# Performance work log

Measured on AMD Instinct MI355X. Metric: run time of the kernel, lower is better.

Reference implementation:

```python
import jax, jax.numpy as jnp
import numpy as np

D_MODEL = 1024
HEADS = 16
D_HEAD = D_MODEL // HEADS
LN_EPS = 1e-6


def setup_inputs() -> dict:
    key = jax.random.key(0)
    ks = jax.random.split(key, 7)
    B, S = 4, 2048
    scale = 1.0 / np.sqrt(D_MODEL)
    return {
        "q": jax.random.normal(ks[0], (B, S, D_MODEL), jnp.float32),
        "k": jax.random.normal(ks[1], (B, S, D_MODEL), jnp.float32),
        "v": jax.random.normal(ks[2], (B, S, D_MODEL), jnp.float32),
        "Wq": jax.random.normal(ks[3], (D_MODEL, D_MODEL), jnp.float32) * scale,
        "Wk": jax.random.normal(ks[4], (D_MODEL, D_MODEL), jnp.float32) * scale,
        "Wv": jax.random.normal(ks[5], (D_MODEL, D_MODEL), jnp.float32) * scale,
        "Wo": jax.random.normal(ks[6], (D_MODEL, D_MODEL), jnp.float32) * scale,
        "ln_gamma": jnp.ones((D_MODEL,), jnp.float32),
        "ln_beta": jnp.zeros((D_MODEL,), jnp.float32),
    }


def reference(q, k, v, Wq, Wk, Wv, Wo, ln_gamma, ln_beta):
    B, S, _ = q.shape
    residual = q
    # torch Linear (no bias): y = x @ W.T
    qh = (q @ Wq.T).reshape(B, S, HEADS, D_HEAD).transpose(0, 2, 1, 3)
    kh = (k @ Wk.T).reshape(B, S, HEADS, D_HEAD).transpose(0, 2, 1, 3)
    vh = (v @ Wv.T).reshape(B, S, HEADS, D_HEAD).transpose(0, 2, 1, 3)
    # scaled dot-product attention (no mask, dropout=0)
    att = jnp.einsum("bhsd,bhtd->bhst", qh, kh) / jnp.sqrt(jnp.float32(D_HEAD))
    att = jax.nn.softmax(att, axis=-1)
    ctx = jnp.einsum("bhst,bhtd->bhsd", att, vh)  # (B,H,S,Dh)
    ctx = ctx.transpose(0, 2, 1, 3).reshape(B, S, D_MODEL)
    out = ctx @ Wo.T
    out = out + residual
    # LayerNorm, eps=1e-6
    mu = out.mean(axis=-1, keepdims=True)
    var = out.var(axis=-1, keepdims=True)
    out = (out - mu) * jax.lax.rsqrt(var + LN_EPS) * ln_gamma + ln_beta
    return out
```

## Files before the change

### kernel.cpp

```cpp
#include <hip/hip_runtime.h>
#include <hip/hip_bf16.h>

#define DEVI __device__ __forceinline__

typedef unsigned int u32;
typedef unsigned short u16;
typedef __bf16 bf16_t;
typedef bf16_t bf16x8 __attribute__((ext_vector_type(8)));
typedef bf16_t bf16x4 __attribute__((ext_vector_type(4)));
typedef float f32x4 __attribute__((ext_vector_type(4)));
typedef u32 u32x4 __attribute__((ext_vector_type(4)));
typedef u32 u32x2 __attribute__((ext_vector_type(2)));

DEVI u16 f2bf(float f) {
    u32 u = __builtin_bit_cast(u32, f);
    u = (u + 0x7FFFu + ((u >> 16) & 1u)) >> 16;
    return (u16)u;
}

DEVI u32 pack2bf(float lo, float hi) {
#if __has_builtin(__builtin_amdgcn_cvt_pk_bf16_f32)
    typedef __bf16 bf16x2_t __attribute__((ext_vector_type(2)));
    return __builtin_bit_cast(u32, __builtin_amdgcn_cvt_pk_bf16_f32(lo, hi));
#else
    return (u32)f2bf(lo) | ((u32)f2bf(hi) << 16);
#endif
}

DEVI float fast_exp2(float x) { return __builtin_amdgcn_exp2f(x); }

DEVI f32x4 mfma16x16x16(bf16x4 a, bf16x4 b, f32x4 c) {
#if __has_builtin(__builtin_amdgcn_mfma_f32_16x16x16bf16_1k)
    typedef short s16x4 __attribute__((ext_vector_type(4)));
    return __builtin_amdgcn_mfma_f32_16x16x16bf16_1k(
        __builtin_bit_cast(s16x4, a), __builtin_bit_cast(s16x4, b), c, 0, 0, 0);
#else
    asm volatile("s_nop 1\n\tv_mfma_f32_16x16x16_bf16 %0, %1, %2, %0\n\ts_nop 7\n\ts_nop 3"
                 : "+v"(c) : "v"(a), "v"(b));
    return c;
#endif
}

typedef __attribute__((address_space(3))) u32 as3_u32;
typedef __attribute__((address_space(1))) u32 as1_u32;

DEVI void gld_lds16(const u16* gsrc, u16* ldst) {
    __builtin_amdgcn_global_load_lds((as1_u32*)gsrc, (as3_u32*)ldst, 16, 0, 0);
}

struct CastArgs {
    const float* src[7];
    u16* dst[7];
    int n[7];
};

__global__ __launch_bounds__(256) void cast_kernel(CastArgs a) {
    int z = blockIdx.y;
    int i = (blockIdx.x * 256 + threadIdx.x) * 8;
    if (i >= a.n[z]) return;
    const float* s = a.src[z] + i;
    float4 f0 = ((const float4*)s)[0];
    float4 f1 = ((const float4*)s)[1];
    u32x4 o;
    o.x = pack2bf(f0.x, f0.y);
    o.y = pack2bf(f0.z, f0.w);
    o.z = pack2bf(f1.x, f1.y);
    o.w = pack2bf(f1.z, f1.w);
    *(u32x4*)(a.dst[z] + i) = o;
}

DEVI void gemm_core(const u16* __restrict__ Ag, const u16* __restrict__ Wg,
                    u16* As, u16* Bs, f32x4 acc[4][4],
                    int tid, int mw, int nw, int q, int cl)
{
    const int K = 1024;
    for (int k0 = 0; k0 < K; k0 += 64) {
        if (k0) __syncthreads();
        #pragma unroll
        for (int pass = 0; pass < 4; ++pass) {
            int id = pass * 256 + tid;
            int r = id >> 3, cp = id & 7, cg = cp ^ (r & 7);
            gld_lds16(Ag + (size_t)r * K + k0 + cg * 8, &As[id * 8]);
            gld_lds16(Wg + (size_t)r * K + k0 + cg * 8, &Bs[id * 8]);
        }
        __syncthreads();
        #pragma unroll
        for (int kh = 0; kh < 2; ++kh) {
            bf16x8 af[4], bfr[4];
            #pragma unroll
            for (int i = 0; i < 4; ++i) {
                int R = mw + i * 16 + cl;
                af[i] = *(const bf16x8*)&As[R * 64 + (((kh * 4 + q) ^ (cl & 7)) * 8)];
            }
            #pragma unroll
            for (int j = 0; j < 4; ++j) {
                int R = nw + j * 16 + cl;
                bfr[j] = *(const bf16x8*)&Bs[R * 64 + (((kh * 4 + q) ^ (cl & 7)) * 8)];
            }
            #pragma unroll
            for (int i = 0; i < 4; ++i)
                #pragma unroll
                for (int j = 0; j < 4; ++j)
                    acc[i][j] = __builtin_amdgcn_mfma_f32_16x16x32_bf16(af[i], bfr[j], acc[i][j], 0, 0, 0);
        }
    }
}

struct QKVArgs { const u16* A[3]; const u16* W[3]; u16* out[3]; };

__global__ __launch_bounds__(256) void qkv_gemm(QKVArgs ga) {
    __shared__ __align__(16) u16 As[128 * 64];
    __shared__ __align__(16) u16 Bs[128 * 64];
    int z = blockIdx.z;
    int tid = threadIdx.x;
    int lane = tid & 63, w = tid >> 6;
    int q = lane >> 4, cl = lane & 15;
    int m0 = blockIdx.y * 128, n0 = blockIdx.x * 128;
    int mw = (w >> 1) * 64, nw = (w & 1) * 64;

    f32x4 acc[4][4] = {};
    const u16* Ag = ga.A[z] + (size_t)m0 * 1024;
    const u16* Wg = ga.W[z] + (size_t)n0 * 1024;
    gemm_core(Ag, Wg, As, Bs, acc, tid, mw, nw, q, cl);

    u16* outb = ga.out[z];
    if (z == 0) {
        const float SC = 0.125f * 1.44269504088896340736f;
        #pragma unroll
        for (int i = 0; i < 4; ++i) {
            int row = m0 + mw + i * 16 + q * 4;
            #pragma unroll
            for (int j = 0; j < 4; ++j) {
                int col = n0 + nw + j * 16 + cl;
                #pragma unroll
                for (int r = 0; r < 4; ++r)
                    outb[(size_t)(row + r) * 1024 + col] = f2bf(acc[i][j][r] * SC);
            }
        }
    } else if (z == 1) {
        #pragma unroll
        for (int i = 0; i < 4; ++i) {
            int row = m0 + mw + i * 16 + q * 4;
            #pragma unroll
            for (int j = 0; j < 4; ++j) {
                int col = n0 + nw + j * 16 + cl;
                #pragma unroll
                for (int r = 0; r < 4; ++r)
                    outb[(size_t)(row + r) * 1024 + col] = f2bf(acc[i][j][r]);
            }
        }
    } else {
        #pragma unroll
        for (int i = 0; i < 4; ++i) {
            int mrow = m0 + mw + i * 16 + q * 4;
            int bb = mrow >> 11, s = mrow & 2047;
            #pragma unroll
            for (int j = 0; j < 4; ++j) {
                int n = n0 + nw + j * 16 + cl;
                ushort4 pk;
                pk.x = f2bf(acc[i][j][0]); pk.y = f2bf(acc[i][j][1]);
                pk.z = f2bf(acc[i][j][2]); pk.w = f2bf(acc[i][j][3]);
                *(ushort4*)&outb[(size_t)(bb * 1024 + n) * 2048 + s] = pk;
            }
        }
    }
}

__global__ __launch_bounds__(256) void gemm_wo(
    const u16* __restrict__ A, const u16* __restrict__ W,
    float* __restrict__ outf, const float* __restrict__ resid)
{
    __shared__ __align__(16) u16 As[128 * 64];
    __shared__ __align__(16) u16 Bs[128 * 64];
    int tid = threadIdx.x;
    int lane = tid & 63, w = tid >> 6;
    int q = lane >> 4, cl = lane & 15;
    int m0 = blockIdx.y * 128, n0 = blockIdx.x * 128;
    int mw = (w >> 1) * 64, nw = (w & 1) * 64;

    f32x4 acc[4][4] = {};
    const u16* Ag = A + (size_t)m0 * 1024;
    const u16* Wg = W + (size_t)n0 * 1024;
    gemm_core(Ag, Wg, As, Bs, acc, tid, mw, nw, q, cl);

    #pragma unroll
    for (int i = 0; i < 4; ++i) {
        int row = m0 + mw + i * 16 + q * 4;
        #pragma unroll
        for (int j = 0; j < 4; ++j) {
            int col = n0 + nw + j * 16 + cl;
            #pragma unroll
            for (int r = 0; r < 4; ++r) {
                size_t idx = (size_t)(row + r) * 1024 + col;
                outf[idx] = acc[i][j][r] + resid[idx];
            }
        }
    }
}

__global__ __launch_bounds__(256, 4) void attn_kernel(
    const u16* __restrict__ Qp, const u16* __restrict__ Kp,
    const u16* __restrict__ Vt, u16* __restrict__ ctx)
{
    __shared__ __align__(16) u16 Ks[128 * 64];
    __shared__ __align__(16) u16 Vs[64 * 128];

    int tid = threadIdx.x;
    int lane = tid & 63, w = tid >> 6;
    int q = lane >> 4, cl = lane & 15;
    int bh = blockIdx.y, b = bh >> 4, h = bh & 15;
    int qt = blockIdx.x;

    const u16* Qg = Qp + (size_t)(b * 2048 + qt * 128) * 1024 + h * 64;
    const u16* Kg = Kp + (size_t)(b * 2048) * 1024 + h * 64;
    const u16* Vg = Vt + (size_t)(b * 1024 + h * 64) * 2048;

    bf16x8 aq[2][2];
    #pragma unroll
    for (int tr = 0; tr < 2; ++tr)
        #pragma unroll
        for (int kk = 0; kk < 2; ++kk)
            aq[tr][kk] = *(const bf16x8*)&Qg[(size_t)(w * 32 + tr * 16 + cl) * 1024 + kk * 32 + q * 8];

    u32x2 ou; ou.x = 0x3F803F80u; ou.y = 0x3F803F80u;
    const bf16x4 ones = __builtin_bit_cast(bf16x4, ou);

    f32x4 oacc[2][4] = {};
    f32x4 lacc[2] = {};

    for (int kt = 0; kt < 16; ++kt) {
        __syncthreads();
        #pragma unroll
        for (int p = 0; p < 4; ++p) {
            int cid = p * 256 + tid;
            int r = cid >> 3, cp = cid & 7, cg = cp ^ (r & 7);
            gld_lds16(Kg + (size_t)(kt * 128 + r) * 1024 + cg * 8, &Ks[cid * 8]);
        }
        #pragma unroll
        for (int p = 0; p < 4; ++p) {
            int cid = p * 256 + tid;
            int r = cid >> 4, cp = cid & 15, cg = cp ^ (r & 15);
            gld_lds16(Vg + (size_t)r * 2048 + kt * 128 + cg * 8, &Vs[cid * 8]);
        }
        __syncthreads();

        bf16x4 pb[2][8];
        #pragma unroll
        for (int rt = 0; rt < 8; ++rt) {
            int kr = rt * 16 + cl;
            bf16x8 kf0 = *(const bf16x8*)&Ks[kr * 64 + ((q) ^ (cl & 7)) * 8];
            bf16x8 kf1 = *(const bf16x8*)&Ks[kr * 64 + ((4 + q) ^ (cl & 7)) * 8];
            #pragma unroll
            for (int tr = 0; tr < 2; ++tr) {
                f32x4 s = {0.f, 0.f, 0.f, 0.f};
                s = __builtin_amdgcn_mfma_f32_16x16x32_bf16(kf0, aq[tr][0], s, 0, 0, 0);
                s = __builtin_amdgcn_mfma_f32_16x16x32_bf16(kf1, aq[tr][1], s, 0, 0, 0);
                float p0 = fast_exp2(s[0]);
                float p1 = fast_exp2(s[1]);
                float p2 = fast_exp2(s[2]);
                float p3 = fast_exp2(s[3]);
                u32x2 pk;
                pk.x = pack2bf(p0, p1);
                pk.y = pack2bf(p2, p3);
                pb[tr][rt] = __builtin_bit_cast(bf16x4, pk);
            }
        }

        #pragma unroll
        for (int nk = 0; nk < 8; ++nk) {
            #pragma unroll
            for (int td = 0; td < 4; ++td) {
                int d = td * 16 + cl;
                int clog = nk * 2 + (q >> 1);
                bf16x4 bv = *(const bf16x4*)&Vs[d * 128 + ((clog ^ cl) * 8) + (q & 1) * 4];
                #pragma unroll
                for (int tr = 0; tr < 2; ++tr)
                    oacc[tr][td] = mfma16x16x16(pb[tr][nk], bv, oacc[tr][td]);
            }
            #pragma unroll
            for (int tr = 0; tr < 2; ++tr)
                lacc[tr] = mfma16x16x16(pb[tr][nk], ones, lacc[tr]);
        }
    }

    u16* Cg = ctx + (size_t)(b * 2048 + qt * 128) * 1024 + h * 64;
    #pragma unroll
    for (int tr = 0; tr < 2; ++tr) {
        #pragma unroll
        for (int r = 0; r < 4; ++r) {
            float ir = 1.f / lacc[tr][r];
            int srow = w * 32 + tr * 16 + q * 4 + r;
            #pragma unroll
            for (int td = 0; td < 4; ++td)
                Cg[(size_t)srow * 1024 + td * 16 + cl] = f2bf(oacc[tr][td][r] * ir);
        }
    }
}

__global__ __launch_bounds__(256) void ln_kernel(float* __restrict__ out,
    const float* __restrict__ gamma, const float* __restrict__ beta)
{
    int r = blockIdx.x, tid = threadIdx.x;
    int lane = tid & 63, w = tid >> 6;
    float* x = out + (size_t)r * 1024;
    float4 v = *(const float4*)&x[tid * 4];
    float s = v.x + v.y + v.z + v.w;
    float ss = v.x * v.x + v.y * v.y + v.z * v.z + v.w * v.w;
    #pragma unroll
    for (int off = 1; off < 64; off <<= 1) {
        s += __shfl_xor(s, off, 64);
        ss += __shfl_xor(ss, off, 64);
    }
    __shared__ float red[8];
    if (lane == 0) { red[w] = s; red[4 + w] = ss; }
    __syncthreads();
    s = red[0] + red[1] + red[2] + red[3];
    ss = red[4] + red[5] + red[6] + red[7];
    float mean = s * (1.f / 1024.f);
    float var = ss * (1.f / 1024.f) - mean * mean;
    float rstd = rsqrtf(var + 1e-6f);
    float4 g = *(const float4*)&gamma[tid * 4];
    float4 bt = *(const float4*)&beta[tid * 4];
    float4 y;
    y.x = (v.x - mean) * rstd * g.x + bt.x;
    y.y = (v.y - mean) * rstd * g.y + bt.y;
    y.z = (v.z - mean) * rstd * g.z + bt.z;
    y.w = (v.w - mean) * rstd * g.w + bt.w;
    *(float4*)&x[tid * 4] = y;
}

extern "C" void kernel_launch(void* const* d_in, const int* in_sizes, int n_in,
                              void* d_out, int out_size, void* d_ws, size_t ws_size,
                              hipStream_t stream) {
    const float* q  = (const float*)d_in[0];
    const float* k  = (const float*)d_in[1];
    const float* v  = (const float*)d_in[2];
    const float* Wq = (const float*)d_in[3];
    const float* Wk = (const float*)d_in[4];
    const float* Wv = (const float*)d_in[5];
    const float* Wo = (const float*)d_in[6];
    const float* gamma = (const float*)d_in[7];
    const float* beta  = (const float*)d_in[8];
    float* out = (float*)d_out;

    u16* qb  = (u16*)d_ws;
    u16* kb  = qb + 8388608;
    u16* vb  = kb + 8388608;
    u16* Wqb = vb + 8388608;
    u16* Wkb = Wqb + 1048576;
    u16* Wvb = Wkb + 1048576;
    u16* Wob = Wvb + 1048576;
    u16* Qp  = Wob + 1048576;
    u16* Kp  = Qp + 8388608;
    u16* Vtb = Kp + 8388608;
    u16* ctx = Vtb + 8388608;

    CastArgs ca;
    ca.src[0] = q;  ca.src[1] = k;  ca.src[2] = v;
    ca.src[3] = Wq; ca.src[4] = Wk; ca.src[5] = Wv; ca.src[6] = Wo;
    ca.dst[0] = qb;  ca.dst[1] = kb;  ca.dst[2] = vb;
    ca.dst[3] = Wqb; ca.dst[4] = Wkb; ca.dst[5] = Wvb; ca.dst[6] = Wob;
    ca.n[0] = ca.n[1] = ca.n[2] = 8388608;
    ca.n[3] = ca.n[4] = ca.n[5] = ca.n[6] = 1048576;

    cast_kernel<<<dim3(4096, 7), 256, 0, stream>>>(ca);

    QKVArgs ga;
    ga.A[0] = qb;  ga.A[1] = kb;  ga.A[2] = vb;
    ga.W[0] = Wqb; ga.W[1] = Wkb; ga.W[2] = Wvb;
    ga.out[0] = Qp; ga.out[1] = Kp; ga.out[2] = Vtb;
    qkv_gemm<<<dim3(8, 64, 3), 256, 0, stream>>>(ga);

    attn_kernel<<<dim3(16, 64), 256, 0, stream>>>(Qp, Kp, Vtb, ctx);

    gemm_wo<<<dim3(8, 64), 256, 0, stream>>>(ctx, Wob, out, q);

    ln_kernel<<<8192, 256, 0, stream>>>(out, gamma, beta);
}
```

Measured before the change: 390.9 us.

## Use 16x16x32 MFMA for PV product via permuted K row loading

Replaces the 16x16x16 bf16 MFMAs in the P·V and row-sum accumulation with 16x16x32 MFMAs. K rows are loaded into LDS with a row permutation so that each lane's exp'd score fragments from two 16-row tiles combine into the 8-element A operand. The permuted layout also makes the V fragment loads a single 16-byte read. This halves the MFMA instruction count for the second GEMM, and s_setprio hints are added around the MFMA groups. The trade-off is more intricate index mapping, which could be a correctness risk.

```diff
diff --git a/kernel.cpp b/kernel.cpp
--- a/kernel.cpp
+++ b/kernel.cpp
@@ -28,18 +28,6 @@
 }
 
 DEVI float fast_exp2(float x) { return __builtin_amdgcn_exp2f(x); }
-
-DEVI f32x4 mfma16x16x16(bf16x4 a, bf16x4 b, f32x4 c) {
-#if __has_builtin(__builtin_amdgcn_mfma_f32_16x16x16bf16_1k)
-    typedef short s16x4 __attribute__((ext_vector_type(4)));
-    return __builtin_amdgcn_mfma_f32_16x16x16bf16_1k(
-        __builtin_bit_cast(s16x4, a), __builtin_bit_cast(s16x4, b), c, 0, 0, 0);
-#else
-    asm volatile("s_nop 1\n\tv_mfma_f32_16x16x16_bf16 %0, %1, %2, %0\n\ts_nop 7\n\ts_nop 3"
-                 : "+v"(c) : "v"(a), "v"(b));
-    return c;
-#endif
-}
 
 typedef __attribute__((address_space(3))) u32 as3_u32;
 typedef __attribute__((address_space(1))) u32 as1_u32;
@@ -198,6 +186,11 @@
     }
 }
 
+
+DEVI int kperm(int r) {
+    return (r & 96) | ((r & 12) << 1) | ((r & 16) >> 2) | (r & 3);
+}
+
 __global__ __launch_bounds__(256, 4) void attn_kernel(
     const u16* __restrict__ Qp, const u16* __restrict__ Kp,
     const u16* __restrict__ Vt, u16* __restrict__ ctx)
@@ -222,8 +215,8 @@
         for (int kk = 0; kk < 2; ++kk)
             aq[tr][kk] = *(const bf16x8*)&Qg[(size_t)(w * 32 + tr * 16 + cl) * 1024 + kk * 32 + q * 8];
 
-    u32x2 ou; ou.x = 0x3F803F80u; ou.y = 0x3F803F80u;
-    const bf16x4 ones = __builtin_bit_cast(bf16x4, ou);
+    u32x4 ou; ou.x = 0x3F803F80u; ou.y = 0x3F803F80u; ou.z = 0x3F803F80u; ou.w = 0x3F803F80u;
+    const bf16x8 ones = __builtin_bit_cast(bf16x8, ou);
 
     f32x4 oacc[2][4] = {};
     f32x4 lacc[2] = {};
@@ -234,7 +227,7 @@
         for (int p = 0; p < 4; ++p) {
             int cid = p * 256 + tid;
             int r = cid >> 3, cp = cid & 7, cg = cp ^ (r & 7);
-            gld_lds16(Kg + (size_t)(kt * 128 + r) * 1024 + cg * 8, &Ks[cid * 8]);
+            gld_lds16(Kg + (size_t)(kt * 128 + kperm(r)) * 1024 + cg * 8, &Ks[cid * 8]);
         }
         #pragma unroll
         for (int p = 0; p < 4; ++p) {
@@ -244,42 +237,48 @@
         }
         __syncthreads();
 
-        bf16x4 pb[2][8];
-        #pragma unroll
-        for (int rt = 0; rt < 8; ++rt) {
-            int kr = rt * 16 + cl;
-            bf16x8 kf0 = *(const bf16x8*)&Ks[kr * 64 + ((q) ^ (cl & 7)) * 8];
-            bf16x8 kf1 = *(const bf16x8*)&Ks[kr * 64 + ((4 + q) ^ (cl & 7)) * 8];
+        bf16x8 pb[2][4];
+        #pragma unroll
+        for (int t = 0; t < 4; ++t) {
+            int krA = t * 32 + cl, krB = t * 32 + 16 + cl;
+            bf16x8 ka0 = *(const bf16x8*)&Ks[krA * 64 + ((q ^ (cl & 7)) * 8)];
+            bf16x8 ka1 = *(const bf16x8*)&Ks[krA * 64 + (((4 + q) ^ (cl & 7)) * 8)];
+            bf16x8 kb0 = *(const bf16x8*)&Ks[krB * 64 + ((q ^ (cl & 7)) * 8)];
+            bf16x8 kb1 = *(const bf16x8*)&Ks[krB * 64 + (((4 + q) ^ (cl & 7)) * 8)];
             #pragma unroll
             for (int tr = 0; tr < 2; ++tr) {
-                f32x4 s = {0.f, 0.f, 0.f, 0.f};
-                s = __builtin_amdgcn_mfma_f32_16x16x32_bf16(kf0, aq[tr][0], s, 0, 0, 0);
-                s = __builtin_amdgcn_mfma_f32_16x16x32_bf16(kf1, aq[tr][1], s, 0, 0, 0);
-                float p0 = fast_exp2(s[0]);
-                float p1 = fast_exp2(s[1]);
-                float p2 = fast_exp2(s[2]);
-                float p3 = fast_exp2(s[3]);
-                u32x2 pk;
-                pk.x = pack2bf(p0, p1);
-                pk.y = pack2bf(p2, p3);
-                pb[tr][rt] = __builtin_bit_cast(bf16x4, pk);
-            }
-        }
-
-        #pragma unroll
-        for (int nk = 0; nk < 8; ++nk) {
+                f32x4 sA = {0.f, 0.f, 0.f, 0.f};
+                f32x4 sB = {0.f, 0.f, 0.f, 0.f};
+                __builtin_amdgcn_s_setprio(1);
+                sA = __builtin_amdgcn_mfma_f32_16x16x32_bf16(ka0, aq[tr][0], sA, 0, 0, 0);
+                sA = __builtin_amdgcn_mfma_f32_16x16x32_bf16(ka1, aq[tr][1], sA, 0, 0, 0);
+                sB = __builtin_amdgcn_mfma_f32_16x16x32_bf16(kb0, aq[tr][0], sB, 0, 0, 0);
+                sB = __builtin_amdgcn_mfma_f32_16x16x32_bf16(kb1, aq[tr][1], sB, 0, 0, 0);
+                __builtin_amdgcn_s_setprio(0);
+                u32x4 pk;
+                pk.x = pack2bf(fast_exp2(sA[0]), fast_exp2(sA[1]));
+                pk.y = pack2bf(fast_exp2(sA[2]), fast_exp2(sA[3]));
+                pk.z = pack2bf(fast_exp2(sB[0]), fast_exp2(sB[1]));
+                pk.w = pack2bf(fast_exp2(sB[2]), fast_exp2(sB[3]));
+                pb[tr][t] = __builtin_bit_cast(bf16x8, pk);
+            }
+        }
+
+        #pragma unroll
+        for (int t = 0; t < 4; ++t) {
             #pragma unroll
             for (int td = 0; td < 4; ++td) {
                 int d = td * 16 + cl;
-                int clog = nk * 2 + (q >> 1);
-                bf16x4 bv = *(const bf16x4*)&Vs[d * 128 + ((clog ^ cl) * 8) + (q & 1) * 4];
-                #pragma unroll
-                for (int tr = 0; tr < 2; ++tr)
-                    oacc[tr][td] = mfma16x16x16(pb[tr][nk], bv, oacc[tr][td]);
-            }
-            #pragma unroll
-            for (int tr = 0; tr < 2; ++tr)
-                lacc[tr] = mfma16x16x16(pb[tr][nk], ones, lacc[tr]);
+                bf16x8 bv = *(const bf16x8*)&Vs[d * 128 + (((t * 4 + q) ^ cl) * 8)];
+                __builtin_amdgcn_s_setprio(1);
+                oacc[0][td] = __builtin_amdgcn_mfma_f32_16x16x32_bf16(pb[0][t], bv, oacc[0][td], 0, 0, 0);
+                oacc[1][td] = __builtin_amdgcn_mfma_f32_16x16x32_bf16(pb[1][t], bv, oacc[1][td], 0, 0, 0);
+                __builtin_amdgcn_s_setprio(0);
+            }
+            __builtin_amdgcn_s_setprio(1);
+            lacc[0] = __builtin_amdgcn_mfma_f32_16x16x32_bf16(pb[0][t], ones, lacc[0], 0, 0, 0);
+            lacc[1] = __builtin_amdgcn_mfma_f32_16x16x32_bf16(pb[1][t], ones, lacc[1], 0, 0, 0);
+            __builtin_amdgcn_s_setprio(0);
         }
     }
 
```

Result: faster. 381.2 us (-2.5%).
